# Optimization experiments

Measured on AMD Instinct MI355X. Metric: run time of the kernel, lower is better.

The kernel has to match this reference:

```python
import jax, jax.numpy as jnp
import numpy as np

N_CLASSES = 80
SCORE_THRESH = 0.3
NMS_THRESH = 0.3
TOPK = 100            # max candidates kept per (image, class) for fixed-shape NMS
MAX_PER_IMAGE = 50
ANCHORS = np.array([[10,13],[16,30],[33,23],[30,61],[62,45],[59,119],
                    [116,90],[156,198],[373,326]], dtype=np.float32)
ANCHOR_MASK = ((6,7,8),(3,4,5),(0,1,2))


def setup_inputs() -> dict:
    key = jax.random.key(0)
    k0, k1, k2 = jax.random.split(key, 3)
    B = 16
    feat0 = jax.random.normal(k0, (B, 255, 19, 19), jnp.float32)
    feat1 = jax.random.normal(k1, (B, 255, 38, 38), jnp.float32)
    feat2 = jax.random.normal(k2, (B, 255, 76, 76), jnp.float32)
    anchors = jnp.asarray(ANCHORS)
    image_shape = jnp.array([480.0, 640.0], jnp.float32)  # (h, w) of original image
    return {"feat0": feat0, "feat1": feat1, "feat2": feat2,
            "anchors": anchors, "image_shape": image_shape}


def _decode_scale(feat, anchors_s, input_hw, image_shape):
    # feat: [B, 3*(5+C), gh, gw] -> boxes [B, gh*gw*3, 4], scores [B, gh*gw*3, C]
    B, _, gh, gw = feat.shape
    fm = feat.reshape(B, 3, 5 + N_CLASSES, gh, gw).transpose(0, 3, 4, 1, 2)  # [B,gh,gw,3,5+C]
    gy, gx = jnp.meshgrid(jnp.arange(gh, dtype=feat.dtype),
                          jnp.arange(gw, dtype=feat.dtype), indexing='ij')
    grid = jnp.stack([gx, gy], -1)[None, :, :, None, :]           # [1,gh,gw,1,2] (x,y)
    box_xy = (jax.nn.sigmoid(fm[..., :2]) + grid) / jnp.array([gh, gw], feat.dtype)
    box_wh = anchors_s[None, None, None, :, :] * jnp.exp(fm[..., 2:4]) / input_hw
    conf = jax.nn.sigmoid(fm[..., 4:5])
    probs = jax.nn.sigmoid(fm[..., 5:])
    # letterbox correction (keras-yolo3 yolo_correct_boxes)
    box_yx = box_xy[..., ::-1]
    box_hw = box_wh[..., ::-1]
    new_shape = jnp.round(image_shape * jnp.min(input_hw / image_shape))
    offset = (input_hw - new_shape) / 2.0 / input_hw
    scale = input_hw / new_shape
    box_yx = (box_yx - offset) * scale
    box_hw = box_hw * scale
    mins = box_yx - box_hw / 2.0
    maxes = box_yx + box_hw / 2.0
    boxes = jnp.concatenate([mins, maxes], -1) * jnp.concatenate([image_shape, image_shape])
    scores = conf * probs
    return boxes.reshape(B, -1, 4), scores.reshape(B, -1, N_CLASSES)


def _iou_matrix(b):  # b: [K,4] as (y1,x1,y2,x2)
    y1, x1, y2, x2 = b[:, 0], b[:, 1], b[:, 2], b[:, 3]
    area = (y2 - y1) * (x2 - x1)
    iy1 = jnp.maximum(y1[:, None], y1[None, :])
    ix1 = jnp.maximum(x1[:, None], x1[None, :])
    iy2 = jnp.minimum(y2[:, None], y2[None, :])
    ix2 = jnp.minimum(x2[:, None], x2[None, :])
    inter = jnp.maximum(iy2 - iy1, 0.0) * jnp.maximum(ix2 - ix1, 0.0)
    return inter / (area[:, None] + area[None, :] - inter + 1e-9)


def _nms_class(boxes, scores):  # boxes [N,4], scores [N] -> dets [TOPK,5] (zero-padded)
    s = jnp.where(scores > SCORE_THRESH, scores, -1.0)
    top_s, idx = jax.lax.top_k(s, TOPK)      # candidates sorted descending
    b = boxes[idx]                            # [TOPK,4]
    iou = _iou_matrix(b)
    valid = top_s > SCORE_THRESH
    ar = jnp.arange(TOPK)
    def body(i, keep):
        active = keep[i] & valid[i]
        sup = active & (iou[i] > NMS_THRESH) & (ar > i)
        return keep & ~sup
    keep = jax.lax.fori_loop(0, TOPK, body, valid)
    dets = jnp.concatenate([b, top_s[:, None]], -1)
    return dets * keep[:, None].astype(b.dtype)


def reference(feat0, feat1, feat2, anchors, image_shape):
    input_hw = jnp.array([feat0.shape[2] * 32, feat0.shape[3] * 32], feat0.dtype)
    boxes_all, scores_all = [], []
    for feat, mask in zip((feat0, feat1, feat2), ANCHOR_MASK):
        bx, sc = _decode_scale(feat, anchors[jnp.array(mask)], input_hw, image_shape)
        boxes_all.append(bx)
        scores_all.append(sc)
    boxes = jnp.concatenate(boxes_all, 1)    # [B,N,4]
    scores = jnp.concatenate(scores_all, 1)  # [B,N,C]
    nms_bc = jax.vmap(jax.vmap(_nms_class, in_axes=(None, 0)), in_axes=(0, 0))
    dets = nms_bc(boxes, scores.transpose(0, 2, 1))  # [B,C,TOPK,5]
    def cap(d):  # keep only top MAX_PER_IMAGE detections per image (by score)
        s = d[..., 4].reshape(-1)
        _, ix = jax.lax.top_k(s, MAX_PER_IMAGE)
        m = jnp.zeros(s.shape, bool).at[ix].set(True)
        return d * m.reshape(N_CLASSES, TOPK, 1).astype(d.dtype)
    return jax.vmap(cap)(dets)
```

## Files before the change

### kernel.cpp

```cpp
#include <hip/hip_runtime.h>
#include <math.h>

#define BATCH 16
#define NCLS 80
#define TOPK 100
#define NBOX 22743
#define NSLOT (NCLS*TOPK)
#define TPAD 22752
#define CAP 1024
#define NQ4 5688
#define NSEG 18
#define NZERO (BATCH*NCLS*256)

__device__ __forceinline__ float sigf(float x){ return 1.0f/(1.0f + expf(-x)); }
__device__ __forceinline__ float fsigf(float x){
    return __builtin_amdgcn_rcpf(1.0f + __expf(-x));
}

#define BIN_OF(sc) ({ int _b = (int)(__float_as_uint(sc)>>16) - 0x3E99; _b < 0 ? 0 : (_b > 255 ? 255 : _b); })

struct Seg { const float* fbase; int a; int P; int qc; int confb; int nb; int lqoff; int tailq; };
__device__ __forceinline__ Seg segdec(int z, const float* f0, const float* f1, const float* f2){
    Seg s;
    if (z < 3){       s.a=z;   s.P=361;  s.qc=91;  s.confb=z*364;                s.nb=z;        s.fbase=f0; s.lqoff=0;      s.tailq=90; }
    else if (z < 6){  int a=z-3; s.a=a;  s.P=1444; s.qc=361; s.confb=1092+a*1444; s.nb=1083+a;  s.fbase=f1; s.lqoff=0;      s.tailq=-1; }
    else { int t=z-6; int a=t>>2, ch=t&3; s.a=a; s.P=5776; s.qc=361;
           s.confb=5424+a*5776+ch*1444;  s.nb=5415+a;  s.fbase=f2; s.lqoff=ch*361; s.tailq=-1; }
    return s;
}

struct QGeo { int s; int a; int p; int P; int conf_off; int nb; bool tail; };
__device__ __forceinline__ QGeo qgeo(int i){
    QGeo g;
    if (i < 273){        g.s=0; g.a=i/91;   int lq=i-g.a*91;   g.P=361;  g.conf_off=g.a*364      + lq*4; g.nb=g.a;      g.p=lq*4; g.tail=(lq==90); }
    else if (i < 1356){  int l=i-273;  g.s=1; g.a=l/361;  int lq=l-g.a*361;  g.P=1444; g.conf_off=1092+g.a*1444+ lq*4; g.nb=1083+g.a; g.p=lq*4; g.tail=false; }
    else {               int l=i-1356; g.s=2; g.a=l/1444; int lq=l-g.a*1444; g.P=5776; g.conf_off=5424+g.a*5776+ lq*4; g.nb=5415+g.a; g.p=lq*4; g.tail=false; }
    return g;
}

__global__ __launch_bounds__(256)
void decode_kernel(const float* __restrict__ f0, const float* __restrict__ f1,
                   const float* __restrict__ f2, const float* __restrict__ anchors,
                   const float* __restrict__ ishape,
                   float* __restrict__ boxes, float* __restrict__ conf2,
                   unsigned* __restrict__ gzero)
{
    int i = blockIdx.x*256 + threadIdx.x;
    int b = blockIdx.y;
    int tot = gridDim.x*gridDim.y*256;
    for (int g = (b*gridDim.x + blockIdx.x)*256 + threadIdx.x; g < NZERO; g += tot)
        gzero[g] = 0u;
    if (i >= NQ4) return;
    QGeo g = qgeo(i);
    const float* f = (g.s==0)?f0:((g.s==1)?f1:f2);
    int G = (g.s==0)?19:((g.s==1)?38:76);
    int abase = (g.s==0)?6:((g.s==1)?3:0);
    const float* fb = f + ((size_t)b*255 + g.a*85)*(size_t)g.P;
    float4 TX = *(const float4*)(fb + (size_t)0*g.P + g.p);
    float4 TY = *(const float4*)(fb + (size_t)1*g.P + g.p);
    float4 TW = *(const float4*)(fb + (size_t)2*g.P + g.p);
    float4 TH = *(const float4*)(fb + (size_t)3*g.P + g.p);
    float4 TC = *(const float4*)(fb + (size_t)4*g.P + g.p);
    const float* txp = (const float*)&TX; const float* typ = (const float*)&TY;
    const float* twp = (const float*)&TW; const float* thp = (const float*)&TH;
    const float* tcp = (const float*)&TC;

    float aw = anchors[(abase+g.a)*2+0];
    float ah = anchors[(abase+g.a)*2+1];
    float ih = ishape[0], iw = ishape[1];
    float mm = fminf(608.0f/ih, 608.0f/iw);
    float nh = rintf(ih*mm), nw = rintf(iw*mm);
    float offy = (608.0f - nh) / 2.0f / 608.0f;
    float offx = (608.0f - nw) / 2.0f / 608.0f;
    float scy = 608.0f/nh, scx = 608.0f/nw;
    float gg = (float)G;
    int valid = g.tail ? 1 : 4;
    float cfout[4] = {0.f, 0.f, 0.f, 0.f};
#pragma unroll
    for (int j=0; j<4; j++){
        if (j < valid){
            int px = g.p + j;
            int yy = px / G, xx = px - yy*G;
            float xn = (sigf(txp[j]) + (float)xx) / gg;
            float yn = (sigf(typ[j]) + (float)yy) / gg;
            float wn = aw * expf(twp[j]) / 608.0f;
            float hn = ah * expf(thp[j]) / 608.0f;
            float y = (yn - offy)*scy;
            float x = (xn - offx)*scx;
            float hh = hn*scy, ww = wn*scx;
            int n = g.nb + 3*px;
            float4 bx;
            bx.x = (y - hh/2.0f)*ih;
            bx.y = (x - ww/2.0f)*iw;
            bx.z = (y + hh/2.0f)*ih;
            bx.w = (x + ww/2.0f)*iw;
            *(float4*)&boxes[((size_t)b*NBOX + n)*4] = bx;
            cfout[j] = sigf(tcp[j]);
        }
    }
    float4 cv; cv.x=cfout[0]; cv.y=cfout[1]; cv.z=cfout[2]; cv.w=cfout[3];
    *(float4*)&conf2[(size_t)b*TPAD + g.conf_off] = cv;
}

template<bool WRITEB>
__global__ __launch_bounds__(256)
void scan_kernel(const float* __restrict__ f0, const float* __restrict__ f1,
                 const float* __restrict__ f2, const float* __restrict__ conf2,
                 unsigned int* __restrict__ ghist, unsigned char* __restrict__ binb)
{
    int cg = blockIdx.x, b = blockIdx.y, z = blockIdx.z, tid = threadIdx.x;
    int c0 = cg*4;
    int bc0 = b*NCLS + c0;
    __shared__ unsigned int h[4][256];
    h[0][tid]=0; h[1][tid]=0; h[2][tid]=0; h[3][tid]=0;
    __syncthreads();
    Seg sg = segdec(z, f0, f1, f2);
    const int P = sg.P, qc = sg.qc;
    const float* cfp = conf2 + (size_t)b*TPAD + sg.confb;
    const float* prb = sg.fbase + ((size_t)b*255 + sg.a*85 + 5 + c0)*(size_t)P + sg.lqoff*4;

    int lqA = tid, lqB = tid + 256;
    bool vA = lqA < qc, vB = lqB < qc;
    float4 cfA, cfB, A0, A1, A2, A3, B0, B1, B2, B3;
    if (vA){
        const float* pA = prb + lqA*4;
        cfA = *(const float4*)(cfp + lqA*4);
        A0 = *(const float4*)pA;         A1 = *(const float4*)(pA + P);
        A2 = *(const float4*)(pA + 2*P); A3 = *(const float4*)(pA + 3*P);
    }
    if (vB){
        const float* pB = prb + lqB*4;
        cfB = *(const float4*)(cfp + lqB*4);
        B0 = *(const float4*)pB;         B1 = *(const float4*)(pB + P);
        B2 = *(const float4*)(pB + 2*P); B3 = *(const float4*)(pB + 3*P);
    }
#define HQUAD(cls, Q, CF, LQ) { \
    float s0 = CF.x*fsigf(Q.x), s1 = CF.y*fsigf(Q.y), s2 = CF.z*fsigf(Q.z), s3 = CF.w*fsigf(Q.w); \
    int b0 = BIN_OF(s0), b1 = BIN_OF(s1), b2 = BIN_OF(s2), b3 = BIN_OF(s3); \
    bool k0 = s0 > 0.2995f, k1 = s1 > 0.2995f, k2 = s2 > 0.2995f, k3 = s3 > 0.2995f; \
    if (k0) atomicAdd(&h[cls][b0], 1u); \
    if (k1) atomicAdd(&h[cls][b1], 1u); \
    if (k2) atomicAdd(&h[cls][b2], 1u); \
    if (k3) atomicAdd(&h[cls][b3], 1u); \
    if (WRITEB){ \
        unsigned ub = (k0 ? (unsigned)(b0+1) : 0u) | ((k1 ? (unsigned)(b1+1) : 0u)<<8) \
                    | ((k2 ? (unsigned)(b2+1) : 0u)<<16) | ((k3 ? (unsigned)(b3+1) : 0u)<<24); \
        *(unsigned*)(binb + (size_t)(bc0+cls)*TPAD + sg.confb + (LQ)*4) = ub; } }
    if (vA){
        if (lqA == sg.tailq){
            A0.y=A0.z=A0.w=-INFINITY; A1.y=A1.z=A1.w=-INFINITY;
            A2.y=A2.z=A2.w=-INFINITY; A3.y=A3.z=A3.w=-INFINITY;
        }
        HQUAD(0, A0, cfA, lqA) HQUAD(1, A1, cfA, lqA) HQUAD(2, A2, cfA, lqA) HQUAD(3, A3, cfA, lqA)
    }
    if (vB){
        HQUAD(0, B0, cfB, lqB) HQUAD(1, B1, cfB, lqB) HQUAD(2, B2, cfB, lqB) HQUAD(3, B3, cfB, lqB)
    }
#undef HQUAD
    __syncthreads();
    size_t hb = ((size_t)bc0)*256 + tid;
    if (h[0][tid]) atomicAdd(&ghist[hb      ], h[0][tid]);
    if (h[1][tid]) atomicAdd(&ghist[hb + 256], h[1][tid]);
    if (h[2][tid]) atomicAdd(&ghist[hb + 512], h[2][tid]);
    if (h[3][tid]) atomicAdd(&ghist[hb + 768], h[3][tid]);
}

__device__ void sortnms_out(float* cs, int* ci, int n, const float* __restrict__ boxes,
                            float* __restrict__ out, int b, int bc, int tid)
{
    int S = 128; while (S < n) S <<= 1;
    for (int t=tid; t<S; t+=256){
        if (t >= n){ cs[t] = -INFINITY; ci[t] = 0x7FFFFFFF; }
    }
    __syncthreads();
    for (int k=2; k<=S; k<<=1){
        for (int j=k>>1; j>0; j>>=1){
            for (int t=tid; t<S; t+=256){
                int ixj = t ^ j;
                if (ixj > t){
                    float s1 = cs[t], s2 = cs[ixj];
                    int   i1 = ci[t], i2 = ci[ixj];
                    bool b2_first = (s2 > s1) || (s2 == s1 && i2 < i1);
                    bool b1_first = (s1 > s2) || (s1 == s2 && i1 < i2);
                    bool desc = ((t & k) == 0);
                    bool sw = desc ? b2_first : b1_first;
                    if (sw){ cs[t]=s2; cs[ixj]=s1; ci[t]=i2; ci[ixj]=i1; }
                }
            }
            __syncthreads();
        }
    }
    int w = tid >> 6, lane = tid & 63;
    if (w == 0){
        int o0 = bc*TOPK;
        int nn = n < TOPK ? n : TOPK;
        float ay1=0.f,ax1=0.f,ay2=0.f,ax2=0.f,aar=0.f,asc=0.f; int ak=0;
        float by1=0.f,bx1=0.f,by2=0.f,bx2=0.f,bar_=0.f,bsc=0.f; int bk=0;
        {
            float s = cs[lane];
            if (s > 0.3f){
                asc = s;
                size_t q = ((size_t)b*NBOX + ci[lane])*4;
                ay1=boxes[q]; ax1=boxes[q+1]; ay2=boxes[q+2]; ax2=boxes[q+3]; ak=1;
            }
            aar = (ay2-ay1)*(ax2-ax1);
        }
        if (lane + 64 < TOPK){
            float s = cs[lane+64];
            if (s > 0.3f){
                bsc = s;
                size_t q = ((size_t)b*NBOX + ci[lane+64])*4;
                by1=boxes[q]; bx1=boxes[q+1]; by2=boxes[q+2]; bx2=boxes[q+3]; bk=1;
            }
            bar_ = (by2-by1)*(bx2-bx1);
        }
        for (int i=0; i<nn; i++){
            float iy1,ix1,iy2,ix2,iar; int ik;
            if (i < 64){
                iy1=__shfl(ay1,i); ix1=__shfl(ax1,i); iy2=__shfl(ay2,i); ix2=__shfl(ax2,i);
                iar=__shfl(aar,i); ik=__shfl(ak,i);
            } else {
                int l = i - 64;
                iy1=__shfl(by1,l); ix1=__shfl(bx1,l); iy2=__shfl(by2,l); ix2=__shfl(bx2,l);
                iar=__shfl(bar_,l); ik=__shfl(bk,l);
            }
            if (ik){
                if (ak && lane > i){
                    float q1=fmaxf(iy1,ay1), q2=fmaxf(ix1,ax1);
                    float q3=fminf(iy2,ay2), q4=fminf(ix2,ax2);
                    float inter = fmaxf(q3-q1,0.0f)*fmaxf(q4-q2,0.0f);
                    float iou = inter/(iar + aar - inter + 1e-9f);
                    if (iou > 0.3f) ak = 0;
                }
                if (bk && lane + 64 > i){
                    float q1=fmaxf(iy1,by1), q2=fmaxf(ix1,bx1);
                    float q3=fminf(iy2,by2), q4=fminf(ix2,bx2);
                    float inter = fmaxf(q3-q1,0.0f)*fmaxf(q4-q2,0.0f);
                    float iou = inter/(iar + bar_ - inter + 1e-9f);
                    if (iou > 0.3f) bk = 0;
                }
            }
        }
        {
            float k = ak ? 1.0f : 0.0f;
            size_t o5 = ((size_t)(o0+lane))*5;
            out[o5+0]=ay1*k; out[o5+1]=ax1*k; out[o5+2]=ay2*k; out[o5+3]=ax2*k; out[o5+4]=asc*k;
        }
        if (lane + 64 < TOPK){
            float k = bk ? 1.0f : 0.0f;
            size_t o5 = ((size_t)(o0+lane+64))*5;
            out[o5+0]=by1*k; out[o5+1]=bx1*k; out[o5+2]=by2*k; out[o5+3]=bx2*k; out[o5+4]=bsc*k;
        }
    }
}

template<bool WITHB>
__global__ __launch_bounds__(256)
void selnms_kernel(const float* __restrict__ f0, const float* __restrict__ f1,
                   const float* __restrict__ f2, const float* __restrict__ conf2,
                   const unsigned char* __restrict__ binb,
                   const unsigned int* __restrict__ ghist,
                   const float* __restrict__ boxes, float* __restrict__ out)
{
    int c = blockIdx.x, b = blockIdx.y, tid = threadIdx.x;
    int bc = b*NCLS + c;
    __shared__ int sufA[256], sufB[256];
    __shared__ float cs[CAP];
    __shared__ int   ci[CAP];
    __shared__ int cnt, TbS;
    if (tid == 0){ cnt = 0; TbS = 0; }
    sufA[tid] = (int)ghist[(size_t)bc*256 + tid];
    __syncthreads();
    int* cur = sufA; int* nxt = sufB;
    for (int d=1; d<256; d<<=1){
        int v = cur[tid] + ((tid+d) < 256 ? cur[tid+d] : 0);
        nxt[tid] = v;
        __syncthreads();
        int* t_ = cur; cur = nxt; nxt = t_;
    }
    if (cur[tid] >= TOPK && (tid == 255 || cur[tid+1] < TOPK)) TbS = tid;
    __syncthreads();
    int gate = TbS - 2; if (gate < 0) gate = 0;

    if (WITHB){
        const uint4* bw = (const uint4*)(binb + (size_t)bc*TPAD);
        for (int i = tid; i < NQ4/4; i += 256){
            uint4 u4 = bw[i];
            unsigned wv[4] = {u4.x, u4.y, u4.z, u4.w};
#pragma unroll
            for (int k=0; k<4; k++){
                unsigned ub = wv[k];
                if (!ub) continue;
                int w = i*4 + k;
                QGeo g = qgeo(w);
                const float* f = (g.s==0)?f0:((g.s==1)?f1:f2);
                const float* pr = f + ((size_t)b*255 + g.a*85 + 5 + c)*(size_t)g.P + g.p;
#pragma unroll
                for (int j=0; j<4; j++){
                    unsigned bj = (ub >> (8*j)) & 0xFFu;
                    if (bj && (int)bj - 1 >= gate){
                        float cf = conf2[(size_t)b*TPAD + w*4 + j];
                        float pv = pr[j];
                        float sc = cf * sigf(pv);
                        int pos = atomicAdd(&cnt, 1);
                        if (pos < CAP){ cs[pos] = sc; ci[pos] = g.nb + 3*(g.p + j); }
                    }
                }
            }
        }
    } else {
        for (int i = tid; i < NQ4; i += 256){
            QGeo g = qgeo(i);
            const float* f = (g.s==0)?f0:((g.s==1)?f1:f2);
            float4 cf4 = *(const float4*)(conf2 + (size_t)b*TPAD + g.conf_off);
            const float* pr = f + ((size_t)b*255 + g.a*85 + 5 + c)*(size_t)g.P + g.p;
            float pv[4];
            if (!g.tail){
                float4 t = *(const float4*)pr;
                pv[0]=t.x; pv[1]=t.y; pv[2]=t.z; pv[3]=t.w;
            } else {
                pv[0] = pr[0]; pv[1] = -INFINITY; pv[2] = -INFINITY; pv[3] = -INFINITY;
            }
            const float* cfp = (const float*)&cf4;
#pragma unroll
            for (int j=0; j<4; j++){
                float st = cfp[j]*fsigf(pv[j]);
                if (st > 0.2995f && BIN_OF(st) >= gate){
                    float sc = cfp[j]*sigf(pv[j]);
                    int pos = atomicAdd(&cnt, 1);
                    if (pos < CAP){ cs[pos] = sc; ci[pos] = g.nb + 3*(g.p + j); }
                }
            }
        }
    }
    __syncthreads();
    int n = cnt; if (n > CAP) n = CAP;
    sortnms_out(cs, ci, n, boxes, out, b, bc, tid);
}

__global__ __launch_bounds__(1024)
void cap_kernel(float* __restrict__ out)
{
    int b = blockIdx.x, tid = threadIdx.x;
    __shared__ unsigned int h[256];
    __shared__ int sufA[256], sufB[256];
    __shared__ float cs[512];
    __shared__ int   ci[512];
    __shared__ int cnt, T50;
    __shared__ unsigned char msk[NSLOT];
    if (tid < 256) h[tid] = 0;
    if (tid == 0){ cnt = 0; T50 = 0; }
    for (int u=tid; u<NSLOT; u+=1024) msk[u] = 0;
    __syncthreads();

    for (int u=tid; u<NSLOT; u+=1024){
        float v = out[((size_t)b*NSLOT + u)*5 + 4];
        if (v > 0.0f) atomicAdd(&h[BIN_OF(v)], 1u);
    }
    __syncthreads();

    if (tid < 256) sufA[tid] = (int)h[tid];
    __syncthreads();
    int* cur = sufA; int* nxt = sufB;
    for (int d=1; d<256; d<<=1){
        if (tid < 256) nxt[tid] = cur[tid] + ((tid+d) < 256 ? cur[tid+d] : 0);
        __syncthreads();
        int* t_ = cur; cur = nxt; nxt = t_;
    }
    if (tid < 256){
        if (cur[tid] >= 50 && (tid == 255 || cur[tid+1] < 50)) T50 = tid;
    }
    __syncthreads();
    int T = T50;

    for (int u=tid; u<NSLOT; u+=1024){
        float v = out[((size_t)b*NSLOT + u)*5 + 4];
        if (v > 0.0f && BIN_OF(v) >= T){
            int pos = atomicAdd(&cnt, 1);
            if (pos < 512){ cs[pos] = v; ci[pos] = u; }
        }
    }
    __syncthreads();
    int n = cnt; if (n > 512) n = 512;
    for (int t=tid; t<512; t+=1024){
        if (t >= n){ cs[t] = -INFINITY; ci[t] = 0x7FFFFFFF; }
    }
    __syncthreads();

    int S = 64; while (S < n) S <<= 1;
    for (int k=2; k<=S; k<<=1){
        for (int j=k>>1; j>0; j>>=1){
            for (int t=tid; t<S; t+=1024){
                int ixj = t ^ j;
                if (ixj > t){
                    float s1 = cs[t], s2 = cs[ixj];
                    int   i1 = ci[t], i2 = ci[ixj];
                    bool b2_first = (s2 > s1) || (s2 == s1 && i2 < i1);
                    bool b1_first = (s1 > s2) || (s1 == s2 && i1 < i2);
                    bool desc = ((t & k) == 0);
                    bool sw = desc ? b2_first : b1_first;
                    if (sw){ cs[t]=s2; cs[ixj]=s1; ci[t]=i2; ci[ixj]=i1; }
                }
            }
            __syncthreads();
        }
    }

    if (tid < 50 && tid < n) msk[ci[tid]] = 1;
    __syncthreads();

    for (int u=tid; u<NSLOT; u+=1024){
        size_t o5 = ((size_t)b*NSLOT + u)*5;
        float v = out[o5 + 4];
        if (v > 0.0f && !msk[u]){
            out[o5+0]=0.f; out[o5+1]=0.f; out[o5+2]=0.f; out[o5+3]=0.f; out[o5+4]=0.f;
        }
    }
}

extern "C" void kernel_launch(void* const* d_in, const int* in_sizes, int n_in,
                              void* d_out, int out_size, void* d_ws, size_t ws_size,
                              hipStream_t stream)
{
    const float* f0 = (const float*)d_in[0];
    const float* f1 = (const float*)d_in[1];
    const float* f2 = (const float*)d_in[2];
    const float* anchors = (const float*)d_in[3];
    const float* ishape  = (const float*)d_in[4];
    float* out = (float*)d_out;

    float* boxes = (float*)d_ws;
    float* conf2 = boxes + (size_t)BATCH*NBOX*4;
    unsigned* ghist = (unsigned*)(conf2 + (size_t)BATCH*TPAD);
    unsigned char* binb = (unsigned char*)(ghist + (size_t)NZERO);

    size_t words = (size_t)BATCH*NBOX*4 + (size_t)BATCH*TPAD + (size_t)NZERO;
    size_t need = words*4 + (size_t)BATCH*NCLS*TPAD;
    bool useB = ws_size >= need;

    dim3 dgrid((NQ4 + 255)/256, BATCH);
    decode_kernel<<<dgrid, 256, 0, stream>>>(f0, f1, f2, anchors, ishape,
                                             boxes, conf2, ghist);

    dim3 hgrid(NCLS/4, BATCH, NSEG);
    if (useB)
        scan_kernel<true><<<hgrid, 256, 0, stream>>>(f0, f1, f2, conf2, ghist, binb);
    else
        scan_kernel<false><<<hgrid, 256, 0, stream>>>(f0, f1, f2, conf2, ghist, binb);

    dim3 sgrid(NCLS, BATCH);
    if (useB)
        selnms_kernel<true><<<sgrid, 256, 0, stream>>>(f0, f1, f2, conf2, binb,
                                                       ghist, boxes, out);
    else
        selnms_kernel<false><<<sgrid, 256, 0, stream>>>(f0, f1, f2, conf2, binb,
                                                        ghist, boxes, out);

    cap_kernel<<<BATCH, 1024, 0, stream>>>(out);
}
```

Before: 126.3 us.

## Split candidate compaction across chunked blocks and parallelize NMS via IoU bitmask

The fused select+sort+NMS kernel is split in two. A compaction kernel spreads each (batch, class) candidate scan over four z-chunks and writes into global per-class buffers using global atomics. A separate sort/NMS kernel then computes the full 100x100 IoU suppression bitmask with all threads, so only a short serial bitmask sweep remains on one thread. This adds parallelism to the scan and the NMS in exchange for an extra launch, global-memory round trips for candidates, and a larger workspace requirement. gcnt must be zeroed beforehand (NZERO was enlarged, presumably so the decode kernel clears it), and candidate order now depends on global atomics, though the sort makes the output deterministic.

```diff
diff --git a/kernel.cpp b/kernel.cpp
--- a/kernel.cpp
+++ b/kernel.cpp
@@ -10,7 +10,9 @@
 #define CAP 1024
 #define NQ4 5688
 #define NSEG 18
-#define NZERO (BATCH*NCLS*256)
+#define NCHK 4
+#define WCHK 356
+#define NZERO (BATCH*NCLS*256 + BATCH*NCLS)
 
 __device__ __forceinline__ float sigf(float x){ return 1.0f/(1.0f + expf(-x)); }
 __device__ __forceinline__ float fsigf(float x){
@@ -165,110 +167,20 @@
     if (h[3][tid]) atomicAdd(&ghist[hb + 768], h[3][tid]);
 }
 
-__device__ void sortnms_out(float* cs, int* ci, int n, const float* __restrict__ boxes,
-                            float* __restrict__ out, int b, int bc, int tid)
-{
-    int S = 128; while (S < n) S <<= 1;
-    for (int t=tid; t<S; t+=256){
-        if (t >= n){ cs[t] = -INFINITY; ci[t] = 0x7FFFFFFF; }
-    }
-    __syncthreads();
-    for (int k=2; k<=S; k<<=1){
-        for (int j=k>>1; j>0; j>>=1){
-            for (int t=tid; t<S; t+=256){
-                int ixj = t ^ j;
-                if (ixj > t){
-                    float s1 = cs[t], s2 = cs[ixj];
-                    int   i1 = ci[t], i2 = ci[ixj];
-                    bool b2_first = (s2 > s1) || (s2 == s1 && i2 < i1);
-                    bool b1_first = (s1 > s2) || (s1 == s2 && i1 < i2);
-                    bool desc = ((t & k) == 0);
-                    bool sw = desc ? b2_first : b1_first;
-                    if (sw){ cs[t]=s2; cs[ixj]=s1; ci[t]=i2; ci[ixj]=i1; }
-                }
-            }
-            __syncthreads();
-        }
-    }
-    int w = tid >> 6, lane = tid & 63;
-    if (w == 0){
-        int o0 = bc*TOPK;
-        int nn = n < TOPK ? n : TOPK;
-        float ay1=0.f,ax1=0.f,ay2=0.f,ax2=0.f,aar=0.f,asc=0.f; int ak=0;
-        float by1=0.f,bx1=0.f,by2=0.f,bx2=0.f,bar_=0.f,bsc=0.f; int bk=0;
-        {
-            float s = cs[lane];
-            if (s > 0.3f){
-                asc = s;
-                size_t q = ((size_t)b*NBOX + ci[lane])*4;
-                ay1=boxes[q]; ax1=boxes[q+1]; ay2=boxes[q+2]; ax2=boxes[q+3]; ak=1;
-            }
-            aar = (ay2-ay1)*(ax2-ax1);
-        }
-        if (lane + 64 < TOPK){
-            float s = cs[lane+64];
-            if (s > 0.3f){
-                bsc = s;
-                size_t q = ((size_t)b*NBOX + ci[lane+64])*4;
-                by1=boxes[q]; bx1=boxes[q+1]; by2=boxes[q+2]; bx2=boxes[q+3]; bk=1;
-            }
-            bar_ = (by2-by1)*(bx2-bx1);
-        }
-        for (int i=0; i<nn; i++){
-            float iy1,ix1,iy2,ix2,iar; int ik;
-            if (i < 64){
-                iy1=__shfl(ay1,i); ix1=__shfl(ax1,i); iy2=__shfl(ay2,i); ix2=__shfl(ax2,i);
-                iar=__shfl(aar,i); ik=__shfl(ak,i);
-            } else {
-                int l = i - 64;
-                iy1=__shfl(by1,l); ix1=__shfl(bx1,l); iy2=__shfl(by2,l); ix2=__shfl(bx2,l);
-                iar=__shfl(bar_,l); ik=__shfl(bk,l);
-            }
-            if (ik){
-                if (ak && lane > i){
-                    float q1=fmaxf(iy1,ay1), q2=fmaxf(ix1,ax1);
-                    float q3=fminf(iy2,ay2), q4=fminf(ix2,ax2);
-                    float inter = fmaxf(q3-q1,0.0f)*fmaxf(q4-q2,0.0f);
-                    float iou = inter/(iar + aar - inter + 1e-9f);
-                    if (iou > 0.3f) ak = 0;
-                }
-                if (bk && lane + 64 > i){
-                    float q1=fmaxf(iy1,by1), q2=fmaxf(ix1,bx1);
-                    float q3=fminf(iy2,by2), q4=fminf(ix2,bx2);
-                    float inter = fmaxf(q3-q1,0.0f)*fmaxf(q4-q2,0.0f);
-                    float iou = inter/(iar + bar_ - inter + 1e-9f);
-                    if (iou > 0.3f) bk = 0;
-                }
-            }
-        }
-        {
-            float k = ak ? 1.0f : 0.0f;
-            size_t o5 = ((size_t)(o0+lane))*5;
-            out[o5+0]=ay1*k; out[o5+1]=ax1*k; out[o5+2]=ay2*k; out[o5+3]=ax2*k; out[o5+4]=asc*k;
-        }
-        if (lane + 64 < TOPK){
-            float k = bk ? 1.0f : 0.0f;
-            size_t o5 = ((size_t)(o0+lane+64))*5;
-            out[o5+0]=by1*k; out[o5+1]=bx1*k; out[o5+2]=by2*k; out[o5+3]=bx2*k; out[o5+4]=bsc*k;
-        }
-    }
-}
-
 template<bool WITHB>
 __global__ __launch_bounds__(256)
-void selnms_kernel(const float* __restrict__ f0, const float* __restrict__ f1,
-                   const float* __restrict__ f2, const float* __restrict__ conf2,
-                   const unsigned char* __restrict__ binb,
-                   const unsigned int* __restrict__ ghist,
-                   const float* __restrict__ boxes, float* __restrict__ out)
-{
-    int c = blockIdx.x, b = blockIdx.y, tid = threadIdx.x;
+void compact3_kernel(const float* __restrict__ f0, const float* __restrict__ f1,
+                     const float* __restrict__ f2, const float* __restrict__ conf2,
+                     const unsigned char* __restrict__ binb,
+                     const unsigned int* __restrict__ ghist,
+                     int* __restrict__ gcnt, float* __restrict__ gsc,
+                     int* __restrict__ gix)
+{
+    int c = blockIdx.x, b = blockIdx.y, z = blockIdx.z, tid = threadIdx.x;
     int bc = b*NCLS + c;
     __shared__ int sufA[256], sufB[256];
-    __shared__ float cs[CAP];
-    __shared__ int   ci[CAP];
-    __shared__ int cnt, TbS;
-    if (tid == 0){ cnt = 0; TbS = 0; }
+    __shared__ int TbS;
+    if (tid == 0) TbS = 0;
     sufA[tid] = (int)ghist[(size_t)bc*256 + tid];
     __syncthreads();
     int* cur = sufA; int* nxt = sufB;
@@ -284,7 +196,9 @@
 
     if (WITHB){
         const uint4* bw = (const uint4*)(binb + (size_t)bc*TPAD);
-        for (int i = tid; i < NQ4/4; i += 256){
+        int ibeg = z*WCHK, iend = (z+1)*WCHK;
+        if (iend > NQ4/4) iend = NQ4/4;
+        for (int i = ibeg + tid; i < iend; i += 256){
             uint4 u4 = bw[i];
             unsigned wv[4] = {u4.x, u4.y, u4.z, u4.w};
 #pragma unroll
@@ -302,14 +216,19 @@
                         float cf = conf2[(size_t)b*TPAD + w*4 + j];
                         float pv = pr[j];
                         float sc = cf * sigf(pv);
-                        int pos = atomicAdd(&cnt, 1);
-                        if (pos < CAP){ cs[pos] = sc; ci[pos] = g.nb + 3*(g.p + j); }
+                        int pos = atomicAdd(&gcnt[bc], 1);
+                        if (pos < CAP){
+                            gsc[(size_t)bc*CAP + pos] = sc;
+                            gix[(size_t)bc*CAP + pos] = g.nb + 3*(g.p + j);
+                        }
                     }
                 }
             }
         }
     } else {
-        for (int i = tid; i < NQ4; i += 256){
+        int qbeg = z*(NQ4/NCHK + 1), qend = qbeg + (NQ4/NCHK + 1);
+        if (qend > NQ4) qend = NQ4;
+        for (int i = qbeg + tid; i < qend; i += 256){
             QGeo g = qgeo(i);
             const float* f = (g.s==0)?f0:((g.s==1)?f1:f2);
             float4 cf4 = *(const float4*)(conf2 + (size_t)b*TPAD + g.conf_off);
@@ -327,15 +246,105 @@
                 float st = cfp[j]*fsigf(pv[j]);
                 if (st > 0.2995f && BIN_OF(st) >= gate){
                     float sc = cfp[j]*sigf(pv[j]);
-                    int pos = atomicAdd(&cnt, 1);
-                    if (pos < CAP){ cs[pos] = sc; ci[pos] = g.nb + 3*(g.p + j); }
+                    int pos = atomicAdd(&gcnt[bc], 1);
+                    if (pos < CAP){
+                        gsc[(size_t)bc*CAP + pos] = sc;
+                        gix[(size_t)bc*CAP + pos] = g.nb + 3*(g.p + j);
+                    }
                 }
             }
         }
     }
-    __syncthreads();
-    int n = cnt; if (n > CAP) n = CAP;
-    sortnms_out(cs, ci, n, boxes, out, b, bc, tid);
+}
+
+__global__ __launch_bounds__(256)
+void sortnms2_kernel(const float* __restrict__ gsc, const int* __restrict__ gix,
+                     const int* __restrict__ gcnt, const float* __restrict__ boxes,
+                     float* __restrict__ out)
+{
+    int c = blockIdx.x, b = blockIdx.y, tid = threadIdx.x;
+    int bc = b*NCLS + c;
+    __shared__ float cs[CAP];
+    __shared__ int   ci[CAP];
+    __shared__ float by1[TOPK], bx1[TOPK], by2[TOPK], bx2[TOPK], bar_[TOPK];
+    __shared__ unsigned sup[TOPK][4];
+    __shared__ unsigned keepw[4];
+    int n = gcnt[bc]; if (n > CAP) n = CAP;
+    for (int t=tid; t<CAP; t+=256){
+        if (t < n){ cs[t] = gsc[(size_t)bc*CAP + t]; ci[t] = gix[(size_t)bc*CAP + t]; }
+        else { cs[t] = -INFINITY; ci[t] = 0x7FFFFFFF; }
+    }
+    if (tid < 4) keepw[tid] = 0u;
+    for (int r=tid; r<TOPK; r+=256){ sup[r][0]=0u; sup[r][1]=0u; sup[r][2]=0u; sup[r][3]=0u; }
+    __syncthreads();
+    int S = 128; while (S < n) S <<= 1;
+    for (int k=2; k<=S; k<<=1){
+        for (int j=k>>1; j>0; j>>=1){
+            for (int t=tid; t<S; t+=256){
+                int ixj = t ^ j;
+                if (ixj > t){
+                    float s1 = cs[t], s2 = cs[ixj];
+                    int   i1 = ci[t], i2 = ci[ixj];
+                    bool b2_first = (s2 > s1) || (s2 == s1 && i2 < i1);
+                    bool b1_first = (s1 > s2) || (s1 == s2 && i1 < i2);
+                    bool desc = ((t & k) == 0);
+                    bool sw = desc ? b2_first : b1_first;
+                    if (sw){ cs[t]=s2; cs[ixj]=s1; ci[t]=i2; ci[ixj]=i1; }
+                }
+            }
+            __syncthreads();
+        }
+    }
+
+    if (tid < TOPK){
+        float s = cs[tid];
+        float y1=0.f,x1=0.f,y2=0.f,x2=0.f;
+        if (s > 0.3f){
+            size_t q = ((size_t)b*NBOX + ci[tid])*4;
+            y1=boxes[q]; x1=boxes[q+1]; y2=boxes[q+2]; x2=boxes[q+3];
+            atomicOr(&keepw[tid>>5], 1u << (tid & 31));
+        }
+        by1[tid]=y1; bx1[tid]=x1; by2[tid]=y2; bx2[tid]=x2;
+        bar_[tid] = (y2-y1)*(x2-x1);
+    }
+    __syncthreads();
+
+    for (int p = tid; p < TOPK*TOPK; p += 256){
+        int i = p / TOPK, j = p - i*TOPK;
+        if (j > i){
+            float q1 = fmaxf(by1[i], by1[j]);
+            float q2 = fmaxf(bx1[i], bx1[j]);
+            float q3 = fminf(by2[i], by2[j]);
+            float q4 = fminf(bx2[i], bx2[j]);
+            float inter = fmaxf(q3-q1, 0.0f)*fmaxf(q4-q2, 0.0f);
+            float iou = inter/(bar_[i] + bar_[j] - inter + 1e-9f);
+            if (iou > 0.3f) atomicOr(&sup[i][j>>5], 1u << (j & 31));
+        }
+    }
+    __syncthreads();
+
+    if (tid == 0){
+        unsigned k0 = keepw[0], k1 = keepw[1], k2 = keepw[2], k3 = keepw[3];
+        for (int i = 0; i < TOPK; i++){
+            uint4 sp = *(const uint4*)sup[i];
+            unsigned kw = (i < 32) ? k0 : ((i < 64) ? k1 : ((i < 96) ? k2 : k3));
+            if (kw & (1u << (i & 31))){
+                k0 &= ~sp.x; k1 &= ~sp.y; k2 &= ~sp.z; k3 &= ~sp.w;
+            }
+        }
+        keepw[0]=k0; keepw[1]=k1; keepw[2]=k2; keepw[3]=k3;
+    }
+    __syncthreads();
+
+    if (tid < TOPK){
+        bool kept = (keepw[tid>>5] >> (tid & 31)) & 1u;
+        size_t o5 = ((size_t)(bc*TOPK + tid))*5;
+        out[o5+0] = kept ? by1[tid] : 0.f;
+        out[o5+1] = kept ? bx1[tid] : 0.f;
+        out[o5+2] = kept ? by2[tid] : 0.f;
+        out[o5+3] = kept ? bx2[tid] : 0.f;
+        out[o5+4] = kept ? cs[tid]  : 0.f;
+    }
 }
 
 __global__ __launch_bounds__(1024)
@@ -432,9 +441,13 @@
     float* boxes = (float*)d_ws;
     float* conf2 = boxes + (size_t)BATCH*NBOX*4;
     unsigned* ghist = (unsigned*)(conf2 + (size_t)BATCH*TPAD);
-    unsigned char* binb = (unsigned char*)(ghist + (size_t)NZERO);
-
-    size_t words = (size_t)BATCH*NBOX*4 + (size_t)BATCH*TPAD + (size_t)NZERO;
+    int* gcnt = (int*)(ghist + (size_t)BATCH*NCLS*256);
+    float* gsc = (float*)(gcnt + BATCH*NCLS);
+    int*   gix = (int*)(gsc + (size_t)BATCH*NCLS*CAP);
+    unsigned char* binb = (unsigned char*)(gix + (size_t)BATCH*NCLS*CAP);
+
+    size_t words = (size_t)BATCH*NBOX*4 + (size_t)BATCH*TPAD + (size_t)NZERO
+                 + 2*(size_t)BATCH*NCLS*CAP;
     size_t need = words*4 + (size_t)BATCH*NCLS*TPAD;
     bool useB = ws_size >= need;
 
@@ -448,13 +461,16 @@
     else
         scan_kernel<false><<<hgrid, 256, 0, stream>>>(f0, f1, f2, conf2, ghist, binb);
 
+    dim3 cgrid(NCLS, BATCH, NCHK);
+    if (useB)
+        compact3_kernel<true><<<cgrid, 256, 0, stream>>>(f0, f1, f2, conf2, binb,
+                                                         ghist, gcnt, gsc, gix);
+    else
+        compact3_kernel<false><<<cgrid, 256, 0, stream>>>(f0, f1, f2, conf2, binb,
+                                                          ghist, gcnt, gsc, gix);
+
     dim3 sgrid(NCLS, BATCH);
-    if (useB)
-        selnms_kernel<true><<<sgrid, 256, 0, stream>>>(f0, f1, f2, conf2, binb,
-                                                       ghist, boxes, out);
-    else
-        selnms_kernel<false><<<sgrid, 256, 0, stream>>>(f0, f1, f2, conf2, binb,
-                                                        ghist, boxes, out);
+    sortnms2_kernel<<<sgrid, 256, 0, stream>>>(gsc, gix, gcnt, boxes, out);
 
     cap_kernel<<<BATCH, 1024, 0, stream>>>(out);
 }
```

Result: slower. 137.1 us (+8.5%).
